# Optimization experiments

Measured on AMD Instinct MI355X. Metric: run time of the kernel, lower is better.

The kernel has to match this reference:

```python
import jax, jax.numpy as jnp
import numpy as np

T, B, S = 32, 64, 64          # tgt_len, batch, src_len
V, E, H, L = 32000, 512, 1024, 2  # vocab, word_vec, rnn_size, layers


def setup_inputs() -> dict:
    key = jax.random.key(0)
    ks = jax.random.split(key, 16)
    s = 0.02
    emb = jax.random.normal(ks[5], (V, E)) * s
    emb = emb.at[0].set(0.0)  # padding_idx=0 row is zero
    return {
        "input": jax.random.randint(ks[0], (T, B), 0, V),
        "h0": jax.random.normal(ks[1], (L, B, H)) * s,
        "c0": jax.random.normal(ks[2], (L, B, H)) * s,
        "context": jax.random.normal(ks[3], (S, B, H)),
        "init_output": jax.random.normal(ks[4], (B, H)) * s,
        "embedding": emb,
        "W_ih0": jax.random.normal(ks[6], (4 * H, E + H)) * s,  # layer0 input = emb + input-feed
        "W_hh0": jax.random.normal(ks[7], (4 * H, H)) * s,
        "b0": jnp.zeros((4 * H,), jnp.float32),
        "W_ih1": jax.random.normal(ks[8], (4 * H, H)) * s,
        "W_hh1": jax.random.normal(ks[9], (4 * H, H)) * s,
        "b1": jnp.zeros((4 * H,), jnp.float32),
        "attn_in_w": jax.random.normal(ks[10], (H, H)) * s,
        "attn_out_w": jax.random.normal(ks[11], (H, 2 * H)) * s,
        "copy_in_w": jax.random.normal(ks[12], (H, H)) * s,
    }


def _lstm_cell(x, h, c, W_ih, W_hh, b):
    g = x @ W_ih.T + h @ W_hh.T + b
    i, f, gg, o = jnp.split(g, 4, axis=-1)  # PyTorch gate order i,f,g,o
    c_new = jax.nn.sigmoid(f) * c + jax.nn.sigmoid(i) * jnp.tanh(gg)
    h_new = jax.nn.sigmoid(o) * jnp.tanh(c_new)
    return h_new, c_new


def _global_attention(in_w, out_w, query, ctx):
    # query: (B,H), ctx: (B,S,H)
    q = query @ in_w.T
    scores = jnp.einsum('bd,bsd->bs', q, ctx)
    a = jax.nn.softmax(scores, axis=-1)
    wctx = jnp.einsum('bs,bsd->bd', a, ctx)
    out = jnp.tanh(jnp.concatenate([wctx, query], axis=-1) @ out_w.T)
    return out, a


def reference(input, h0, c0, context, init_output, embedding,
              W_ih0, W_hh0, b0, W_ih1, W_hh1, b1,
              attn_in_w, attn_out_w, copy_in_w):
    ctx = jnp.transpose(context, (1, 0, 2))  # (B,S,H)
    emb = embedding[input]                    # (T,B,E)

    def step(carry, emb_t):
        h, c, out_feed = carry
        x = jnp.concatenate([emb_t, out_feed], axis=-1)  # input feed
        h0n, c0n = _lstm_cell(x, h[0], c[0], W_ih0, W_hh0, b0)
        h1n, c1n = _lstm_cell(h0n, h[1], c[1], W_ih1, W_hh1, b1)
        out, a_std = _global_attention(attn_in_w, attn_out_w, h1n, ctx)
        # copy attention: only the weights are kept by the original module
        qc = out @ copy_in_w.T
        a_copy = jax.nn.softmax(jnp.einsum('bd,bsd->bs', qc, ctx), axis=-1)
        new_carry = (jnp.stack([h0n, h1n]), jnp.stack([c0n, c1n]), out)
        return new_carry, (out, a_std, a_copy)

    (h_T, c_T, _), (outputs, attn_std, attn_copy) = jax.lax.scan(
        step, (h0, c0, init_output), emb)
    return outputs, (h_T, c_T), attn_std, attn_copy
```

## Files before the change

### kernel.cpp

```cpp
#include <hip/hip_runtime.h>

typedef unsigned short u16;
typedef unsigned int   u32;
typedef __attribute__((ext_vector_type(8))) __bf16 bfrag;
typedef __attribute__((ext_vector_type(4))) float  f32x4;
typedef __attribute__((ext_vector_type(2))) u32    u32x2;
typedef __attribute__((ext_vector_type(4))) u32    u32x4;

#define DEVI static __device__ __forceinline__

#define ST2SC(p, v)    asm volatile("global_store_short %0, %1, off sc0 sc1"   :: "v"(p), "v"(v) : "memory")
#define ST4SC(p, v)    asm volatile("global_store_dword %0, %1, off sc0 sc1"   :: "v"(p), "v"(v) : "memory")
#define ST8SC(p, v)    asm volatile("global_store_dwordx2 %0, %1, off sc0 sc1" :: "v"(p), "v"(v) : "memory")
#define ST16SC(p, v)   asm volatile("global_store_dwordx4 %0, %1, off sc0 sc1" :: "v"(p), "v"(v) : "memory")
#define VMFLUSH()      asm volatile("s_waitcnt vmcnt(0)" ::: "memory")

constexpr long OUT_OFF = 0;
constexpr long HT_OFF  = 2097152;
constexpr long CT_OFF  = 2228224;
constexpr long AS_OFF  = 2359296;
constexpr long AC_OFF  = 2490368;

constexpr long WAO_O   = 0;
constexpr long CTX_O   = 4194304;
constexpr long OFR_O   = 0;
constexpr long H0R_O   = 4194304;
constexpr long H1R_O   = 8388608;
constexpr long WAI_O   = 12582912;
constexpr long WC_O    = 14680064;
constexpr long CTXW_O  = 16777216;
constexpr long CTXWC_O = 25165824;
constexpr long CTXOT_O = 33554432;
constexpr long EBF_O   = 41943040;
constexpr long OF0_O   = 44040192;
constexpr long H00_O   = 44171264;
constexpr long H10_O   = 44302336;
constexpr long AB_O    = 44433408;
constexpr long AFLAG_O = 44957696;
constexpr long BAR_O   = 44965888;

constexpr int W0LDS_O = 0;
constexpr int W1LDS_O = 81920;
constexpr int SCR_O   = 147456;
constexpr int SCR2_O  = 156160;

struct KParams {
  const int* input; const float* h0; const float* c0; const float* context;
  const float* init_output; const float* embedding;
  const float* W_ih0; const float* W_hh0; const float* b0;
  const float* W_ih1; const float* W_hh1; const float* b1;
  const float* attn_in; const float* attn_out; const float* copy_in;
  float* out; char* ws;
};

DEVI float bf2f(u16 u) { u32 x = ((u32)u) << 16; return __builtin_bit_cast(float, x); }
DEVI u16 f2bf(float f) {
  u32 x = __builtin_bit_cast(u32, f);
  u32 r = x + 0x7fffu + ((x >> 16) & 1u);
  return (u16)(r >> 16);
}
DEVI void cvtc_sc(const float* s, char* d) {
  float4 v = *(const float4*)s;
  u32x2 u;
  u[0] = (u32)f2bf(v.x) | ((u32)f2bf(v.y) << 16);
  u[1] = (u32)f2bf(v.z) | ((u32)f2bf(v.w) << 16);
  ST8SC(d, u);
}
DEVI float sigm(float x)  { return 1.f / (1.f + __expf(-x)); }
DEVI float tanh_(float x) { return 1.f - 2.f / (__expf(2.f * x) + 1.f); }
DEVI f32x4 mfma16(bfrag a, bfrag b, f32x4 c) {
  return __builtin_amdgcn_mfma_f32_16x16x32_bf16(a, b, c, 0, 0, 0);
}
DEVI u32 fragoff(int m, int k) {
  return (u32)((((k >> 5) * 4 + (m >> 4)) * 64 + ((k >> 3) & 3) * 16 + (m & 15)) * 16 + (k & 7) * 2);
}
DEVI char* of_slot(char* w, int s) { return w + (s ? OFR_O + (long)(s - 1) * 131072 : OF0_O); }
DEVI char* h0_slot(char* w, int s) { return w + (s ? H0R_O + (long)(s - 1) * 131072 : H00_O); }
DEVI char* h1_slot(char* w, int s) { return w + (s ? H1R_O + (long)(s - 1) * 131072 : H10_O); }

DEVI void pollflags(u32* flags, u32 gen) {
  int t = threadIdx.x;
  for (;;) {
    u32 a = __hip_atomic_load(&flags[t],       __ATOMIC_RELAXED, __HIP_MEMORY_SCOPE_AGENT);
    u32 b = __hip_atomic_load(&flags[64 + t],  __ATOMIC_RELAXED, __HIP_MEMORY_SCOPE_AGENT);
    u32 c = __hip_atomic_load(&flags[128 + t], __ATOMIC_RELAXED, __HIP_MEMORY_SCOPE_AGENT);
    u32 d = __hip_atomic_load(&flags[192 + t], __ATOMIC_RELAXED, __HIP_MEMORY_SCOPE_AGENT);
    if (__all((a >= gen) && (b >= gen) && (c >= gen) && (d >= gen))) break;
  }
}
DEVI void barr_arrive(u32* flags, u32 gen) {
  VMFLUSH();
  __syncthreads();
  if (threadIdx.x == 0)
    __hip_atomic_store(&flags[blockIdx.x], gen, __ATOMIC_RELAXED, __HIP_MEMORY_SCOPE_AGENT);
}
DEVI void barr_wait(u32* flags, u32 gen) {
  u32* bc = flags + 320;
  if (blockIdx.x == 128) {
    if (threadIdx.x < 64) pollflags(flags, gen);
    __syncthreads();
    if (threadIdx.x == 0)
      __hip_atomic_store(bc, gen, __ATOMIC_RELAXED, __HIP_MEMORY_SCOPE_AGENT);
  } else {
    if (threadIdx.x == 0) {
      while (__hip_atomic_load(bc, __ATOMIC_RELAXED, __HIP_MEMORY_SCOPE_AGENT) < gen) {}
    }
  }
  __syncthreads();
  asm volatile("" ::: "memory");
}
DEVI void gsync_fence(u32* flags, u32 gen) {
  __syncthreads();
  if (threadIdx.x == 0) {
    __builtin_amdgcn_fence(__ATOMIC_RELEASE, "agent");
    __hip_atomic_store(&flags[blockIdx.x], gen, __ATOMIC_RELAXED, __HIP_MEMORY_SCOPE_AGENT);
  }
  if (threadIdx.x < 64) pollflags(flags, gen);
  if (threadIdx.x == 0) __builtin_amdgcn_fence(__ATOMIC_ACQUIRE, "agent");
  __syncthreads();
}

template<int N4>
DEVI void gseg(f32x4& acc, const char* Af, int kkA0, int mt, int lane,
               const char* W, int wRowK, int kkW0, int brow, int ke) {
  const u32 sw = (u32)((brow & 7) << 4);
#pragma unroll
  for (int g = 0; g < N4; ++g) {
#pragma unroll
    for (int q = 0; q < 4; ++q) {
      const char* pa = Af + ((((kkA0 + g * 4 + q) * 4 + mt) * 64 + lane) << 4);
      bfrag av = *(const bfrag*)pa;
      int kkW = kkW0 + g * 4 + q;
      u32 off = ((u32)(brow * wRowK + kkW * 32 + ke) * 2) ^ sw;
      acc = mfma16(av, *(const bfrag*)(W + off), acc);
    }
  }
}

DEVI void scr_store(float* scr, int slot, f32x4 acc) {
  const int lane = threadIdx.x & 63;
#pragma unroll
  for (int r = 0; r < 4; ++r)
    scr[slot * 272 + ((lane >> 4) * 4 + r) * 17 + (lane & 15)] = acc[r];
}

DEVI void pointwise64(int bid, const float* scr, const float* bias, float (&cst)[4], char* hfrag) {
  const int m = threadIdx.x;
  const int mt = m >> 4, ml = m & 15;
  u32 hp0 = 0, hp1 = 0;
#pragma unroll
  for (int u = 0; u < 4; ++u) {
    const int j = bid * 4 + u;
    float g0 = scr[(mt*2)*272 + ml*17 + u]      + scr[(mt*2+1)*272 + ml*17 + u]      + bias[j];
    float g1 = scr[(mt*2)*272 + ml*17 + 4 + u]  + scr[(mt*2+1)*272 + ml*17 + 4 + u]  + bias[1024 + j];
    float g2 = scr[(mt*2)*272 + ml*17 + 8 + u]  + scr[(mt*2+1)*272 + ml*17 + 8 + u]  + bias[2048 + j];
    float g3 = scr[(mt*2)*272 + ml*17 + 12 + u] + scr[(mt*2+1)*272 + ml*17 + 12 + u] + bias[3072 + j];
    float cn = sigm(g1) * cst[u] + sigm(g0) * tanh_(g2);
    cst[u] = cn;
    u32 hb = (u32)f2bf(sigm(g3) * tanh_(cn));
    if (u == 0) hp0 = hb; else if (u == 1) hp0 |= hb << 16;
    else if (u == 2) hp1 = hb; else hp1 |= hb << 16;
  }
  u32x2 v; v[0] = hp0; v[1] = hp1;
  ST8SC(hfrag + fragoff(m, bid * 4), v);
}

DEVI void copyattn_step(int b, int tau, const u16* CtxWc, const float* outp,
                        float* xch, float* dout) {
  const int tid = threadIdx.x, lane = tid & 63, w = tid >> 6;
  float ov[16];
  {
    const float4* op = (const float4*)(outp + (long)tau * 65536 + b * 1024 + lane * 16);
#pragma unroll
    for (int i = 0; i < 4; ++i) {
      float4 v = op[i];
      ov[4 * i] = v.x; ov[4 * i + 1] = v.y; ov[4 * i + 2] = v.z; ov[4 * i + 3] = v.w;
    }
  }
  const u16* cwb = CtxWc + (long)b * 65536;
#pragma unroll
  for (int si = 0; si < 8; ++si) {
    int s = w * 8 + si;
    const u32* u = (const u32*)(cwb + (long)s * 1024 + lane * 16);
    float acc = 0.f;
#pragma unroll
    for (int i = 0; i < 8; ++i) {
      u32 x = u[i];
      acc += ov[2 * i] * bf2f((u16)(x & 0xffff));
      acc += ov[2 * i + 1] * bf2f((u16)(x >> 16));
    }
#pragma unroll
    for (int off = 32; off; off >>= 1) acc += __shfl_down(acc, off, 64);
    if (lane == 0) xch[s] = acc;
  }
  __syncthreads();
  if (w == 0) {
    float v = xch[lane];
    float mx = v;
#pragma unroll
    for (int off = 32; off; off >>= 1) mx = fmaxf(mx, __shfl_xor(mx, off, 64));
    float e = __expf(v - mx);
    float sm = e;
#pragma unroll
    for (int off = 32; off; off >>= 1) sm += __shfl_xor(sm, off, 64);
    dout[AC_OFF + (long)tau * 4096 + b * 64 + lane] = e / sm;
  }
}

DEVI void ctxw_gemm(int mt, const u16* Ctx, const u16* Wm, u16* dst) {
  const int tid = threadIdx.x, lane = tid & 63, w = tid >> 6;
  const int arow = mt * 16 + (lane & 15);
  const int ke = (lane >> 4) * 8;
#pragma unroll
  for (int i = 0; i < 8; ++i) {
    int nt = w * 8 + i;
    const u16* A = Ctx + (long)arow * 1024 + ke;
    const u16* B = Wm + (long)(nt * 16 + (lane & 15)) * 1024 + ke;
    f32x4 acc = {0.f, 0.f, 0.f, 0.f};
    for (int kk = 0; kk < 1024; kk += 32)
      acc = mfma16(*(const bfrag*)(A + kk), *(const bfrag*)(B + kk), acc);
#pragma unroll
    for (int r = 0; r < 4; ++r)
      ST2SC((char*)(dst + (long)(mt * 16 + (lane >> 4) * 4 + r) * 1024 + nt * 16 + (lane & 15)),
            (u32)f2bf(acc[r]));
  }
}

DEVI void ctxo_gemm(int bid, const u16* Ctx, const u16* Wao, u16* dst) {
  const int tid = threadIdx.x, lane = tid & 63, w = tid >> 6;
  const int arow = bid * 16 + (lane & 15);
  const int ke = (lane >> 4) * 8;
  const int b = bid >> 2, s0 = (bid & 3) * 16 + (lane >> 4) * 4;
#pragma unroll
  for (int i = 0; i < 8; ++i) {
    int nt = w * 8 + i;
    int j = nt * 16 + (lane & 15);
    const u16* A = Ctx + (long)arow * 1024 + ke;
    const u16* B = Wao + (long)j * 2048 + ke;
    f32x4 acc = {0.f, 0.f, 0.f, 0.f};
    for (int kk = 0; kk < 1024; kk += 32)
      acc = mfma16(*(const bfrag*)(A + kk), *(const bfrag*)(B + kk), acc);
    u32x2 q;
    q[0] = (u32)f2bf(acc[0]) | ((u32)f2bf(acc[1]) << 16);
    q[1] = (u32)f2bf(acc[2]) | ((u32)f2bf(acc[3]) << 16);
    ST8SC((char*)(dst + ((long)(b * 1024 + j) * 64 + s0)), q);
  }
}

__global__ __launch_bounds__(512, 1) void decoder_kernel(KParams p) {
  extern __shared__ char smem[];
  char*  W0   = smem + W0LDS_O;
  char*  W1   = smem + W1LDS_O;
  float* scr  = (float*)(smem + SCR_O);
  float* scr2 = (float*)(smem + SCR2_O);

  char* wsb = p.ws;
  u16* Wao   = (u16*)(wsb + WAO_O);
  u16* Wai   = (u16*)(wsb + WAI_O);
  u16* Wc    = (u16*)(wsb + WC_O);
  u16* Ctx   = (u16*)(wsb + CTX_O);
  u16* CtxW  = (u16*)(wsb + CTXW_O);
  u16* CtxWc = (u16*)(wsb + CTXWC_O);
  u16* CtxOT = (u16*)(wsb + CTXOT_O);
  u32* bar   = (u32*)(wsb + BAR_O);

  const int bid = blockIdx.x, tid = threadIdx.x;
  const int lane = tid & 63, w = tid >> 6;
  const long gtid = (long)bid * 512 + tid, NT = 256l * 512;
  u32 gen = 1;

  {
    float* tile = (float*)smem;
    for (int pass = 0; pass < 2; ++pass) {
      const float* src = pass ? p.copy_in : p.attn_in;
      u16* dst = pass ? Wc : Wai;
      int tr = bid >> 4, tc = bid & 15;
      {
        int r = tid >> 3, c = (tid & 7) * 8;
        const float4* s4 = (const float4*)(src + (long)(tr * 64 + r) * 1024 + tc * 64 + c);
        float4 a = s4[0], b = s4[1];
        float* tp = tile + r * 69 + c;
        tp[0] = a.x; tp[1] = a.y; tp[2] = a.z; tp[3] = a.w;
        tp[4] = b.x; tp[5] = b.y; tp[6] = b.z; tp[7] = b.w;
      }
      __syncthreads();
      {
        int r2 = tid >> 3, c2 = (tid & 7) * 8;
        u32x4 q;
#pragma unroll
        for (int i = 0; i < 4; ++i) {
          float lo = tile[(c2 + 2 * i) * 69 + r2];
          float hi = tile[(c2 + 2 * i + 1) * 69 + r2];
          q[i] = (u32)f2bf(lo) | ((u32)f2bf(hi) << 16);
        }
        ST16SC((char*)(dst + (long)(tc * 64 + r2) * 1024 + tr * 64 + c2), q);
      }
      __syncthreads();
    }
  }

  for (int i = tid; i < 5120; i += 512) {
    int row = i / 320, k = (i % 320) * 8;
    int R = (row >> 2) * 1024 + bid * 4 + (row & 3);
    const float* src = (k < 1536) ? (p.W_ih0 + (long)R * 1536 + k)
                                  : (p.W_hh0 + (long)R * 1024 + (k - 1536));
    float4 a = *(const float4*)src, b = *(const float4*)(src + 4);
    uint4 q;
    q.x = (u32)f2bf(a.x) | ((u32)f2bf(a.y) << 16);
    q.y = (u32)f2bf(a.z) | ((u32)f2bf(a.w) << 16);
    q.z = (u32)f2bf(b.x) | ((u32)f2bf(b.y) << 16);
    q.w = (u32)f2bf(b.z) | ((u32)f2bf(b.w) << 16);
    u32 off = ((u32)(row * 2560 + k) * 2) ^ ((u32)((row & 7) << 4));
    *(uint4*)(W0 + off) = q;
  }
  for (int i = tid; i < 4096; i += 512) {
    int row = i / 256, k = (i % 256) * 8;
    int R = (row >> 2) * 1024 + bid * 4 + (row & 3);
    const float* src = (k < 1024) ? (p.W_ih1 + (long)R * 1024 + k)
                                  : (p.W_hh1 + (long)R * 1024 + (k - 1024));
    float4 a = *(const float4*)src, b = *(const float4*)(src + 4);
    uint4 q;
    q.x = (u32)f2bf(a.x) | ((u32)f2bf(a.y) << 16);
    q.y = (u32)f2bf(a.z) | ((u32)f2bf(a.w) << 16);
    q.z = (u32)f2bf(b.x) | ((u32)f2bf(b.y) << 16);
    q.w = (u32)f2bf(b.z) | ((u32)f2bf(b.w) << 16);
    u32 off = ((u32)(row * 2048 + k) * 2) ^ ((u32)((row & 7) << 4));
    *(uint4*)(W1 + off) = q;
  }

  for (long i = gtid; i < 524288; i += NT) cvtc_sc(p.attn_out + i * 4, (char*)(Wao + i * 4));
  for (long i = gtid; i < 1048576; i += NT) {
    long b = i >> 14, s = (i >> 8) & 63, kq = i & 255;
    cvtc_sc(p.context + ((s * 64 + b) * 1024 + kq * 4), (char*)(Ctx + i * 4));
  }
  for (long i = gtid; i < 262144; i += NT) {
    long row = i >> 7; long t = row >> 6, b = row & 63;
    long k0 = (i & 127) * 4;
    long tok = p.input[row];
    cvtc_sc(p.embedding + tok * 512 + k0, wsb + EBF_O + t * 65536 + fragoff((int)b, (int)k0));
  }
  for (long i = gtid; i < 16384; i += NT) {
    long b = i >> 8, k0 = (i & 255) * 4;
    cvtc_sc(p.init_output + i * 4, of_slot(wsb, 0) + fragoff((int)b, (int)k0));
  }
  for (long i = gtid; i < 32768; i += NT) {
    long l = i >> 14, rem = i & 16383, b = rem >> 8, k0 = (rem & 255) * 4;
    cvtc_sc(p.h0 + i * 4, (l ? h1_slot(wsb, 0) : h0_slot(wsb, 0)) + fragoff((int)b, (int)k0));
  }

  float cR0[4] = {0.f, 0.f, 0.f, 0.f}, cR1[4] = {0.f, 0.f, 0.f, 0.f};
  if (tid < 64) {
#pragma unroll
    for (int u = 0; u < 4; ++u) {
      cR0[u] = p.c0[(long)tid * 1024 + bid * 4 + u];
      cR1[u] = p.c0[65536 + (long)tid * 1024 + bid * 4 + u];
    }
  }

  gsync_fence(bar, gen); ++gen;

  ctxw_gemm(bid, Ctx, Wai, CtxW);
  ctxw_gemm(bid, Ctx, Wc, CtxWc);
  ctxo_gemm(bid, Ctx, Wao, CtxOT);
  gsync_fence(bar, gen); ++gen;

  const int xcd = bid & 7, idx = bid >> 3;
  const int ntP4 = xcd * 8 + (idx & 7), mtP4 = idx >> 3;
  const int browP4 = ntP4 * 16 + (lane & 15);
  const int ke_ = (lane >> 4) * 8;
  bfrag waoreg[4];
#pragma unroll
  for (int q = 0; q < 4; ++q)
    waoreg[q] = *(const bfrag*)(Wao + (long)browP4 * 2048 + 1024 + (w * 4 + q) * 32 + ke_);

  const int mt_ = w & 3, kh_ = w >> 2;
  const int brow_ = lane & 15;

  f32x4 accP1 = {0.f, 0.f, 0.f, 0.f}, accP2;
  {
    const char* E0  = wsb + EBF_O;
    const char* H0p = h0_slot(wsb, 0);
    if (kh_ == 0) {
      gseg<2>(accP1, E0,  0,  mt_, lane, W0, 2560, 0,  brow_, ke_);
      gseg<4>(accP1, H0p, 0,  mt_, lane, W0, 2560, 48, brow_, ke_);
    } else {
      gseg<2>(accP1, E0,  8,  mt_, lane, W0, 2560, 8,  brow_, ke_);
      gseg<4>(accP1, H0p, 16, mt_, lane, W0, 2560, 64, brow_, ke_);
    }
  }

  for (int t = 0; t < 32; ++t) {
    const char* OFc   = of_slot(wsb, t);
    char*       Hb0cF = h0_slot(wsb, t + 1);
    char*       Hb1cF = h1_slot(wsb, t + 1);
    const char* Hb1pF = h1_slot(wsb, t);
    char*       ABt   = wsb + AB_O + (long)t * 16384;

    {
      f32x4 acc = accP1;
      if (kh_ == 0) gseg<4>(acc, OFc, 0,  mt_, lane, W0, 2560, 16, brow_, ke_);
      else          gseg<4>(acc, OFc, 16, mt_, lane, W0, 2560, 32, brow_, ke_);
      scr_store(scr, mt_ * 2 + kh_, acc);
      __syncthreads();
      if (tid < 64) pointwise64(bid, scr, p.b0, cR0, Hb0cF);
    }
    barr_arrive(bar, gen);
    accP2 = f32x4{0.f, 0.f, 0.f, 0.f};
    if (kh_ == 0) gseg<4>(accP2, Hb1pF, 0,  mt_, lane, W1, 2048, 32, brow_, ke_);
    else          gseg<4>(accP2, Hb1pF, 16, mt_, lane, W1, 2048, 48, brow_, ke_);
    barr_wait(bar, gen); ++gen;

    {
      f32x4 acc = accP2;
      if (kh_ == 0) gseg<4>(acc, Hb0cF, 0,  mt_, lane, W1, 2048, 0,  brow_, ke_);
      else          gseg<4>(acc, Hb0cF, 16, mt_, lane, W1, 2048, 16, brow_, ke_);
      scr_store(scr, mt_ * 2 + kh_, acc);
      __syncthreads();
      if (tid < 64) pointwise64(bid, scr, p.b1, cR1, Hb1cF);
    }
    barr_arrive(bar, gen);
    accP1 = f32x4{0.f, 0.f, 0.f, 0.f};
    {
      const char* En = wsb + EBF_O + (long)((t + 1) & 31) * 65536;
      if (kh_ == 0) {
        gseg<2>(accP1, En,    0,  mt_, lane, W0, 2560, 0,  brow_, ke_);
        gseg<2>(accP1, Hb0cF, 0,  mt_, lane, W0, 2560, 48, brow_, ke_);
      } else {
        gseg<2>(accP1, En,    8,  mt_, lane, W0, 2560, 8,  brow_, ke_);
        gseg<2>(accP1, Hb0cF, 16, mt_, lane, W0, 2560, 64, brow_, ke_);
      }
    }
    barr_wait(bar, gen); ++gen;

    if (bid < 64) {
      const int b = bid;
      float h1v[16];
      {
        int k0 = lane * 16;
        const u32* hp0 = (const u32*)(Hb1cF + fragoff(b, k0));
        const u32* hp1 = (const u32*)(Hb1cF + fragoff(b, k0 + 8));
        u32 uu[8] = {hp0[0], hp0[1], hp0[2], hp0[3], hp1[0], hp1[1], hp1[2], hp1[3]};
#pragma unroll
        for (int i = 0; i < 8; ++i) {
          h1v[2 * i]     = bf2f((u16)(uu[i] & 0xffff));
          h1v[2 * i + 1] = bf2f((u16)(uu[i] >> 16));
        }
      }
      const u16* cwb = CtxW + (long)b * 65536;
#pragma unroll
      for (int si = 0; si < 8; ++si) {
        int s = w * 8 + si;
        const u32* u = (const u32*)(cwb + (long)s * 1024 + lane * 16);
        float acc = 0.f;
#pragma unroll
        for (int i = 0; i < 8; ++i) {
          u32 x = u[i];
          acc += h1v[2 * i] * bf2f((u16)(x & 0xffff));
          acc += h1v[2 * i + 1] * bf2f((u16)(x >> 16));
        }
#pragma unroll
        for (int off = 32; off; off >>= 1) acc += __shfl_down(acc, off, 64);
        if (lane == 0) scr2[s] = acc;
      }
      __syncthreads();
      if (w == 0) {
        float v = scr2[lane];
        float mx = v;
#pragma unroll
        for (int off = 32; off; off >>= 1) mx = fmaxf(mx, __shfl_xor(mx, off, 64));
        float e = __expf(v - mx);
        float sm = e;
#pragma unroll
        for (int off = 32; off; off >>= 1) sm += __shfl_xor(sm, off, 64);
        float a = e / sm;
        ST4SC(ABt + (u32)(b * 64 + lane) * 4, __builtin_bit_cast(u32, a));
        ST4SC((char*)(p.out + AS_OFF + (long)t * 4096 + b * 64 + lane), __builtin_bit_cast(u32, a));
        VMFLUSH();
        if (lane == 0)
          ST4SC(wsb + AFLAG_O + ((u32)t * 64 + b) * 4, 1u);
      }
      __syncthreads();
    }
    {
      const char* bp = Hb1cF;
      bfrag h0_ = *(const bfrag*)(bp + ((((w * 4 + 0) * 4 + mtP4) * 64 + lane) << 4));
      bfrag h1_ = *(const bfrag*)(bp + ((((w * 4 + 1) * 4 + mtP4) * 64 + lane) << 4));
      bfrag h2_ = *(const bfrag*)(bp + ((((w * 4 + 2) * 4 + mtP4) * 64 + lane) << 4));
      bfrag h3_ = *(const bfrag*)(bp + ((((w * 4 + 3) * 4 + mtP4) * 64 + lane) << 4));
      f32x4 a4 = {0.f, 0.f, 0.f, 0.f};
      a4 = mfma16(h0_, waoreg[0], a4);
      a4 = mfma16(h1_, waoreg[1], a4);
      a4 = mfma16(h2_, waoreg[2], a4);
      a4 = mfma16(h3_, waoreg[3], a4);
      scr_store(scr, w, a4);
    }
    if (bid >= 192 && t > 0)
      copyattn_step(bid - 192, t - 1, CtxWc, p.out, scr2, p.out);

    {
      const int pair = tid >> 1, half = tid & 1;
      const int m_l = pair >> 4, j_l = pair & 15;
      const int b = mtP4 * 16 + m_l, j = ntP4 * 16 + j_l;
      u32 cpr[16];
      {
        const u32* cp = (const u32*)(CtxOT + ((long)(b * 1024 + j) * 64 + half * 32));
#pragma unroll
        for (int i = 0; i < 16; ++i) cpr[i] = cp[i];
      }
      if (tid < 16) {
        const u32* fp = (const u32*)(wsb + AFLAG_O + ((u32)t * 64 + mtP4 * 16 + tid) * 4);
        while (__hip_atomic_load(fp, __ATOMIC_RELAXED, __HIP_MEMORY_SCOPE_AGENT) == 0) {}
      }
      __syncthreads();
      {
        int b0i = tid >> 6, s0i = tid & 63;
        int b1i = (tid + 512) >> 6;
        scr2[tid]       = *(const float*)(ABt + (u32)(((mtP4 * 16 + b0i) * 64 + s0i)) * 4);
        scr2[tid + 512] = *(const float*)(ABt + (u32)(((mtP4 * 16 + b1i) * 64 + s0i)) * 4);
      }
      __syncthreads();
      const float* al = scr2 + m_l * 64 + half * 32;
      float acc = 0.f;
#pragma unroll
      for (int i = 0; i < 16; ++i) {
        u32 x = cpr[i];
        acc += al[2 * i] * bf2f((u16)(x & 0xffff));
        acc += al[2 * i + 1] * bf2f((u16)(x >> 16));
      }
      float v = acc + __shfl_xor(acc, 1, 64);
      if (half == 0) {
        float h1p = 0.f;
#pragma unroll
        for (int q = 0; q < 8; ++q) h1p += scr[q * 272 + m_l * 17 + j_l];
        v = tanh_(v + h1p);
        ST4SC((char*)(p.out + (long)t * 65536 + b * 1024 + j), __builtin_bit_cast(u32, v));
        u32 hv = (u32)f2bf(v);
        ST2SC(of_slot(wsb, t + 1) + fragoff(b, j), hv);
      }
    }
    barr_arrive(bar, gen);
    if (kh_ == 0) gseg<2>(accP1, Hb0cF, 8,  mt_, lane, W0, 2560, 56, brow_, ke_);
    else          gseg<2>(accP1, Hb0cF, 24, mt_, lane, W0, 2560, 72, brow_, ke_);
    barr_wait(bar, gen); ++gen;
  }

  if (tid < 64) {
#pragma unroll
    for (int u = 0; u < 4; ++u) {
      int j = bid * 4 + u;
      p.out[CT_OFF + (long)tid * 1024 + j]         = cR0[u];
      p.out[CT_OFF + 65536 + (long)tid * 1024 + j] = cR1[u];
    }
  }
  if (tid < 256) {
    int u = tid >> 6, m = tid & 63, j = bid * 4 + u;
    u16 a0 = *(const u16*)(h0_slot(wsb, 32) + fragoff(m, j));
    u16 a1 = *(const u16*)(h1_slot(wsb, 32) + fragoff(m, j));
    p.out[HT_OFF + (long)m * 1024 + j]         = bf2f(a0);
    p.out[HT_OFF + 65536 + (long)m * 1024 + j] = bf2f(a1);
  }

  if (bid >= 192) {
    __syncthreads();
    copyattn_step(bid - 192, 31, CtxWc, p.out, scr2, p.out);
  }
}

extern "C" void kernel_launch(void* const* d_in, const int* in_sizes, int n_in,
                              void* d_out, int out_size, void* d_ws, size_t ws_size,
                              hipStream_t stream) {
  KParams p;
  p.input       = (const int*)d_in[0];
  p.h0          = (const float*)d_in[1];
  p.c0          = (const float*)d_in[2];
  p.context     = (const float*)d_in[3];
  p.init_output = (const float*)d_in[4];
  p.embedding   = (const float*)d_in[5];
  p.W_ih0       = (const float*)d_in[6];
  p.W_hh0       = (const float*)d_in[7];
  p.b0          = (const float*)d_in[8];
  p.W_ih1       = (const float*)d_in[9];
  p.W_hh1       = (const float*)d_in[10];
  p.b1          = (const float*)d_in[11];
  p.attn_in     = (const float*)d_in[12];
  p.attn_out    = (const float*)d_in[13];
  p.copy_in     = (const float*)d_in[14];
  p.out         = (float*)d_out;
  p.ws          = (char*)d_ws;

  (void)hipFuncSetAttribute((const void*)decoder_kernel,
                            hipFuncAttributeMaxDynamicSharedMemorySize, 160256);
  (void)hipMemsetAsync((char*)d_ws + AB_O, 0, 534528, stream);
  void* args[] = { &p };
  (void)hipLaunchCooperativeKernel((void*)decoder_kernel, dim3(256), dim3(512),
                                   args, 160256, stream);
}
```

Baseline: 1.534 ms.

## Replace grid-wide barriers with per-chunk dataflow counters and dedicated attention blocks

Removes the per-step global arrive/wait barriers. In their place, each block increments per-chunk counters after producing h0, h1 and output-feed slices, and consumers poll only the chunks they need. The output-projection tiles are redistributed so the first 64 blocks handle attention scores exclusively and the other blocks take one or two projection tiles each. The software pipelining of the next step's embedding and hidden partial GEMMs across barriers is dropped. This trades global barrier latency for finer-grained waits, which may let layers and steps overlap, at the cost of more atomics, polling traffic and some load imbalance from the dual-tile blocks.

```diff
diff --git a/kernel.cpp b/kernel.cpp
--- a/kernel.cpp
+++ b/kernel.cpp
@@ -37,7 +37,10 @@
 constexpr long H10_O   = 44302336;
 constexpr long AB_O    = 44433408;
 constexpr long AFLAG_O = 44957696;
-constexpr long BAR_O   = 44965888;
+constexpr long H0C_O   = 44965888;
+constexpr long H1C_O   = 45033472;
+constexpr long OFC_O   = 45101056;
+constexpr long BAR_O   = 45168640;
 
 constexpr int W0LDS_O = 0;
 constexpr int W1LDS_O = 81920;
@@ -78,6 +81,20 @@
 DEVI char* h0_slot(char* w, int s) { return w + (s ? H0R_O + (long)(s - 1) * 131072 : H00_O); }
 DEVI char* h1_slot(char* w, int s) { return w + (s ? H1R_O + (long)(s - 1) * 131072 : H10_O); }
 
+DEVI u32* cntb(char* w, long base, int slot) { return (u32*)(w + base + (long)slot * 2048); }
+DEVI void cnt_add(u32* c) {
+  (void)__hip_atomic_fetch_add(c, 1u, __ATOMIC_RELAXED, __HIP_MEMORY_SCOPE_AGENT);
+}
+template<int N>
+DEVI void poll_chunks(const u32* base, int c0) {
+  const int lane = threadIdx.x & 63;
+  const u32* p = base + (u32)(c0 + (lane & (N - 1))) * 16;
+  for (;;) {
+    u32 v = __hip_atomic_load(p, __ATOMIC_RELAXED, __HIP_MEMORY_SCOPE_AGENT);
+    if (__all(v >= 8u)) break;
+  }
+}
+
 DEVI void pollflags(u32* flags, u32 gen) {
   int t = threadIdx.x;
   for (;;) {
@@ -87,27 +104,6 @@
     u32 d = __hip_atomic_load(&flags[192 + t], __ATOMIC_RELAXED, __HIP_MEMORY_SCOPE_AGENT);
     if (__all((a >= gen) && (b >= gen) && (c >= gen) && (d >= gen))) break;
   }
-}
-DEVI void barr_arrive(u32* flags, u32 gen) {
-  VMFLUSH();
-  __syncthreads();
-  if (threadIdx.x == 0)
-    __hip_atomic_store(&flags[blockIdx.x], gen, __ATOMIC_RELAXED, __HIP_MEMORY_SCOPE_AGENT);
-}
-DEVI void barr_wait(u32* flags, u32 gen) {
-  u32* bc = flags + 320;
-  if (blockIdx.x == 128) {
-    if (threadIdx.x < 64) pollflags(flags, gen);
-    __syncthreads();
-    if (threadIdx.x == 0)
-      __hip_atomic_store(bc, gen, __ATOMIC_RELAXED, __HIP_MEMORY_SCOPE_AGENT);
-  } else {
-    if (threadIdx.x == 0) {
-      while (__hip_atomic_load(bc, __ATOMIC_RELAXED, __HIP_MEMORY_SCOPE_AGENT) < gen) {}
-    }
-  }
-  __syncthreads();
-  asm volatile("" ::: "memory");
 }
 DEVI void gsync_fence(u32* flags, u32 gen) {
   __syncthreads();
@@ -225,7 +221,6 @@
             (u32)f2bf(acc[r]));
   }
 }
-
 DEVI void ctxo_gemm(int bid, const u16* Ctx, const u16* Wao, u16* dst) {
   const int tid = threadIdx.x, lane = tid & 63, w = tid >> 6;
   const int arow = bid * 16 + (lane & 15);
@@ -245,6 +240,63 @@
     q[1] = (u32)f2bf(acc[2]) | ((u32)f2bf(acc[3]) << 16);
     ST8SC((char*)(dst + ((long)(b * 1024 + j) * 64 + s0)), q);
   }
+}
+
+DEVI void p4_tile(int t, int mt, int nt, const bfrag (&waoreg)[4],
+                  const char* H1n, char* wsb, const u16* CtxOT,
+                  float* scr, float* scr2, float* outp) {
+  const int tid = threadIdx.x, lane = tid & 63, w = tid >> 6;
+  poll_chunks<4>(cntb(wsb, H1C_O, t + 1), w * 4);
+  {
+    bfrag h0_ = *(const bfrag*)(H1n + ((((w * 4 + 0) * 4 + mt) * 64 + lane) << 4));
+    bfrag h1_ = *(const bfrag*)(H1n + ((((w * 4 + 1) * 4 + mt) * 64 + lane) << 4));
+    bfrag h2_ = *(const bfrag*)(H1n + ((((w * 4 + 2) * 4 + mt) * 64 + lane) << 4));
+    bfrag h3_ = *(const bfrag*)(H1n + ((((w * 4 + 3) * 4 + mt) * 64 + lane) << 4));
+    f32x4 a4 = {0.f, 0.f, 0.f, 0.f};
+    a4 = mfma16(h0_, waoreg[0], a4);
+    a4 = mfma16(h1_, waoreg[1], a4);
+    a4 = mfma16(h2_, waoreg[2], a4);
+    a4 = mfma16(h3_, waoreg[3], a4);
+    scr_store(scr, w, a4);
+  }
+  char* ABt = wsb + AB_O + (long)t * 16384;
+  if (tid < 16) {
+    const u32* fp = (const u32*)(wsb + AFLAG_O + ((u32)t * 64 + mt * 16 + tid) * 4);
+    while (__hip_atomic_load(fp, __ATOMIC_RELAXED, __HIP_MEMORY_SCOPE_AGENT) == 0) {}
+  }
+  __syncthreads();
+  {
+    int b0i = tid >> 6, s0i = tid & 63;
+    int b1i = (tid + 512) >> 6;
+    scr2[tid]       = *(const float*)(ABt + (u32)(((mt * 16 + b0i) * 64 + s0i)) * 4);
+    scr2[tid + 512] = *(const float*)(ABt + (u32)(((mt * 16 + b1i) * 64 + s0i)) * 4);
+  }
+  __syncthreads();
+  const int pair = tid >> 1, half = tid & 1;
+  const int m_l = pair >> 4, j_l = pair & 15;
+  const int b = mt * 16 + m_l, j = nt * 16 + j_l;
+  const u32* cp = (const u32*)(CtxOT + ((long)(b * 1024 + j) * 64 + half * 32));
+  const float* al = scr2 + m_l * 64 + half * 32;
+  float acc = 0.f;
+#pragma unroll
+  for (int i = 0; i < 16; ++i) {
+    u32 x = cp[i];
+    acc += al[2 * i] * bf2f((u16)(x & 0xffff));
+    acc += al[2 * i + 1] * bf2f((u16)(x >> 16));
+  }
+  float v = acc + __shfl_xor(acc, 1, 64);
+  if (half == 0) {
+    float h1p = 0.f;
+#pragma unroll
+    for (int q = 0; q < 8; ++q) h1p += scr[q * 272 + m_l * 17 + j_l];
+    v = tanh_(v + h1p);
+    ST4SC((char*)(outp + (long)t * 65536 + b * 1024 + j), __builtin_bit_cast(u32, v));
+    u32 hv = (u32)f2bf(v);
+    ST2SC(of_slot(wsb, t + 1) + fragoff(b, j), hv);
+  }
+  VMFLUSH();
+  __syncthreads();
+  if (tid == 0) cnt_add(cntb(wsb, OFC_O, t + 1) + (nt >> 1) * 16);
 }
 
 __global__ __launch_bounds__(512, 1) void decoder_kernel(KParams p) {
@@ -364,81 +416,75 @@
   ctxo_gemm(bid, Ctx, Wao, CtxOT);
   gsync_fence(bar, gen); ++gen;
 
-  const int xcd = bid & 7, idx = bid >> 3;
-  const int ntP4 = xcd * 8 + (idx & 7), mtP4 = idx >> 3;
-  const int browP4 = ntP4 * 16 + (lane & 15);
+  const bool isP3 = bid < 64;
+  const int tbase = bid - 64;
+  const bool dual = !isP3 && tbase < 64;
+  int mtP4 = 0, ntP4 = 0;
+  if (!isP3) {
+    int vidx = tbase >> 3;
+    mtP4 = vidx >> 3;
+    ntP4 = (tbase & 7) * 8 + (vidx & 7);
+  }
   const int ke_ = (lane >> 4) * 8;
   bfrag waoreg[4];
-#pragma unroll
-  for (int q = 0; q < 4; ++q)
-    waoreg[q] = *(const bfrag*)(Wao + (long)browP4 * 2048 + 1024 + (w * 4 + q) * 32 + ke_);
+  if (!isP3) {
+    const int browP4 = ntP4 * 16 + (lane & 15);
+#pragma unroll
+    for (int q = 0; q < 4; ++q)
+      waoreg[q] = *(const bfrag*)(Wao + (long)browP4 * 2048 + 1024 + (w * 4 + q) * 32 + ke_);
+  }
 
   const int mt_ = w & 3, kh_ = w >> 2;
   const int brow_ = lane & 15;
 
-  f32x4 accP1 = {0.f, 0.f, 0.f, 0.f}, accP2;
-  {
-    const char* E0  = wsb + EBF_O;
-    const char* H0p = h0_slot(wsb, 0);
-    if (kh_ == 0) {
-      gseg<2>(accP1, E0,  0,  mt_, lane, W0, 2560, 0,  brow_, ke_);
-      gseg<4>(accP1, H0p, 0,  mt_, lane, W0, 2560, 48, brow_, ke_);
-    } else {
-      gseg<2>(accP1, E0,  8,  mt_, lane, W0, 2560, 8,  brow_, ke_);
-      gseg<4>(accP1, H0p, 16, mt_, lane, W0, 2560, 64, brow_, ke_);
-    }
-  }
-
   for (int t = 0; t < 32; ++t) {
-    const char* OFc   = of_slot(wsb, t);
-    char*       Hb0cF = h0_slot(wsb, t + 1);
-    char*       Hb1cF = h1_slot(wsb, t + 1);
-    const char* Hb1pF = h1_slot(wsb, t);
-    char*       ABt   = wsb + AB_O + (long)t * 16384;
+    const char* OFc = of_slot(wsb, t);
+    const char* H0c = h0_slot(wsb, t);
+    char*       H0n = h0_slot(wsb, t + 1);
+    char*       H1n = h1_slot(wsb, t + 1);
+    const char* H1c = h1_slot(wsb, t);
 
     {
-      f32x4 acc = accP1;
+      f32x4 acc = {0.f, 0.f, 0.f, 0.f};
+      const char* En = wsb + EBF_O + (long)t * 65536;
+      if (kh_ == 0) gseg<2>(acc, En, 0, mt_, lane, W0, 2560, 0, brow_, ke_);
+      else          gseg<2>(acc, En, 8, mt_, lane, W0, 2560, 8, brow_, ke_);
+      if (t > 0) poll_chunks<16>(cntb(wsb, OFC_O, t), kh_ * 16);
       if (kh_ == 0) gseg<4>(acc, OFc, 0,  mt_, lane, W0, 2560, 16, brow_, ke_);
       else          gseg<4>(acc, OFc, 16, mt_, lane, W0, 2560, 32, brow_, ke_);
+      if (t > 0) poll_chunks<16>(cntb(wsb, H0C_O, t), kh_ * 16);
+      if (kh_ == 0) gseg<4>(acc, H0c, 0,  mt_, lane, W0, 2560, 48, brow_, ke_);
+      else          gseg<4>(acc, H0c, 16, mt_, lane, W0, 2560, 64, brow_, ke_);
       scr_store(scr, mt_ * 2 + kh_, acc);
       __syncthreads();
-      if (tid < 64) pointwise64(bid, scr, p.b0, cR0, Hb0cF);
-    }
-    barr_arrive(bar, gen);
-    accP2 = f32x4{0.f, 0.f, 0.f, 0.f};
-    if (kh_ == 0) gseg<4>(accP2, Hb1pF, 0,  mt_, lane, W1, 2048, 32, brow_, ke_);
-    else          gseg<4>(accP2, Hb1pF, 16, mt_, lane, W1, 2048, 48, brow_, ke_);
-    barr_wait(bar, gen); ++gen;
+      if (tid < 64) { pointwise64(bid, scr, p.b0, cR0, H0n); VMFLUSH(); }
+      __syncthreads();
+      if (tid == 0) cnt_add(cntb(wsb, H0C_O, t + 1) + (bid >> 3) * 16);
+    }
 
     {
-      f32x4 acc = accP2;
-      if (kh_ == 0) gseg<4>(acc, Hb0cF, 0,  mt_, lane, W1, 2048, 0,  brow_, ke_);
-      else          gseg<4>(acc, Hb0cF, 16, mt_, lane, W1, 2048, 16, brow_, ke_);
+      f32x4 acc = {0.f, 0.f, 0.f, 0.f};
+      poll_chunks<16>(cntb(wsb, H0C_O, t + 1), kh_ * 16);
+      if (kh_ == 0) gseg<4>(acc, H0n, 0,  mt_, lane, W1, 2048, 0,  brow_, ke_);
+      else          gseg<4>(acc, H0n, 16, mt_, lane, W1, 2048, 16, brow_, ke_);
+      if (t > 0) poll_chunks<16>(cntb(wsb, H1C_O, t), kh_ * 16);
+      if (kh_ == 0) gseg<4>(acc, H1c, 0,  mt_, lane, W1, 2048, 32, brow_, ke_);
+      else          gseg<4>(acc, H1c, 16, mt_, lane, W1, 2048, 48, brow_, ke_);
       scr_store(scr, mt_ * 2 + kh_, acc);
       __syncthreads();
-      if (tid < 64) pointwise64(bid, scr, p.b1, cR1, Hb1cF);
-    }
-    barr_arrive(bar, gen);
-    accP1 = f32x4{0.f, 0.f, 0.f, 0.f};
-    {
-      const char* En = wsb + EBF_O + (long)((t + 1) & 31) * 65536;
-      if (kh_ == 0) {
-        gseg<2>(accP1, En,    0,  mt_, lane, W0, 2560, 0,  brow_, ke_);
-        gseg<2>(accP1, Hb0cF, 0,  mt_, lane, W0, 2560, 48, brow_, ke_);
-      } else {
-        gseg<2>(accP1, En,    8,  mt_, lane, W0, 2560, 8,  brow_, ke_);
-        gseg<2>(accP1, Hb0cF, 16, mt_, lane, W0, 2560, 64, brow_, ke_);
-      }
-    }
-    barr_wait(bar, gen); ++gen;
-
-    if (bid < 64) {
+      if (tid < 64) { pointwise64(bid, scr, p.b1, cR1, H1n); VMFLUSH(); }
+      __syncthreads();
+      if (tid == 0) cnt_add(cntb(wsb, H1C_O, t + 1) + (bid >> 3) * 16);
+    }
+
+    if (isP3) {
       const int b = bid;
+      poll_chunks<32>(cntb(wsb, H1C_O, t + 1), 0);
       float h1v[16];
       {
         int k0 = lane * 16;
-        const u32* hp0 = (const u32*)(Hb1cF + fragoff(b, k0));
-        const u32* hp1 = (const u32*)(Hb1cF + fragoff(b, k0 + 8));
+        const u32* hp0 = (const u32*)(H1n + fragoff(b, k0));
+        const u32* hp1 = (const u32*)(H1n + fragoff(b, k0 + 8));
         u32 uu[8] = {hp0[0], hp0[1], hp0[2], hp0[3], hp1[0], hp1[1], hp1[2], hp1[3]};
 #pragma unroll
         for (int i = 0; i < 8; ++i) {
@@ -473,77 +519,32 @@
 #pragma unroll
         for (int off = 32; off; off >>= 1) sm += __shfl_xor(sm, off, 64);
         float a = e / sm;
-        ST4SC(ABt + (u32)(b * 64 + lane) * 4, __builtin_bit_cast(u32, a));
+        ST4SC(wsb + AB_O + (long)t * 16384 + (u32)(b * 64 + lane) * 4, __builtin_bit_cast(u32, a));
         ST4SC((char*)(p.out + AS_OFF + (long)t * 4096 + b * 64 + lane), __builtin_bit_cast(u32, a));
         VMFLUSH();
         if (lane == 0)
           ST4SC(wsb + AFLAG_O + ((u32)t * 64 + b) * 4, 1u);
       }
       __syncthreads();
-    }
-    {
-      const char* bp = Hb1cF;
-      bfrag h0_ = *(const bfrag*)(bp + ((((w * 4 + 0) * 4 + mtP4) * 64 + lane) << 4));
-      bfrag h1_ = *(const bfrag*)(bp + ((((w * 4 + 1) * 4 + mtP4) * 64 + lane) << 4));
-      bfrag h2_ = *(const bfrag*)(bp + ((((w * 4 + 2) * 4 + mtP4) * 64 + lane) << 4));
-      bfrag h3_ = *(const bfrag*)(bp + ((((w * 4 + 3) * 4 + mtP4) * 64 + lane) << 4));
-      f32x4 a4 = {0.f, 0.f, 0.f, 0.f};
-      a4 = mfma16(h0_, waoreg[0], a4);
-      a4 = mfma16(h1_, waoreg[1], a4);
-      a4 = mfma16(h2_, waoreg[2], a4);
-      a4 = mfma16(h3_, waoreg[3], a4);
-      scr_store(scr, w, a4);
-    }
-    if (bid >= 192 && t > 0)
-      copyattn_step(bid - 192, t - 1, CtxWc, p.out, scr2, p.out);
-
-    {
-      const int pair = tid >> 1, half = tid & 1;
-      const int m_l = pair >> 4, j_l = pair & 15;
-      const int b = mtP4 * 16 + m_l, j = ntP4 * 16 + j_l;
-      u32 cpr[16];
-      {
-        const u32* cp = (const u32*)(CtxOT + ((long)(b * 1024 + j) * 64 + half * 32));
-#pragma unroll
-        for (int i = 0; i < 16; ++i) cpr[i] = cp[i];
-      }
-      if (tid < 16) {
-        const u32* fp = (const u32*)(wsb + AFLAG_O + ((u32)t * 64 + mtP4 * 16 + tid) * 4);
-        while (__hip_atomic_load(fp, __ATOMIC_RELAXED, __HIP_MEMORY_SCOPE_AGENT) == 0) {}
-      }
-      __syncthreads();
-      {
-        int b0i = tid >> 6, s0i = tid & 63;
-        int b1i = (tid + 512) >> 6;
-        scr2[tid]       = *(const float*)(ABt + (u32)(((mtP4 * 16 + b0i) * 64 + s0i)) * 4);
-        scr2[tid + 512] = *(const float*)(ABt + (u32)(((mtP4 * 16 + b1i) * 64 + s0i)) * 4);
-      }
-      __syncthreads();
-      const float* al = scr2 + m_l * 64 + half * 32;
-      float acc = 0.f;
-#pragma unroll
-      for (int i = 0; i < 16; ++i) {
-        u32 x = cpr[i];
-        acc += al[2 * i] * bf2f((u16)(x & 0xffff));
-        acc += al[2 * i + 1] * bf2f((u16)(x >> 16));
-      }
-      float v = acc + __shfl_xor(acc, 1, 64);
-      if (half == 0) {
-        float h1p = 0.f;
-#pragma unroll
-        for (int q = 0; q < 8; ++q) h1p += scr[q * 272 + m_l * 17 + j_l];
-        v = tanh_(v + h1p);
-        ST4SC((char*)(p.out + (long)t * 65536 + b * 1024 + j), __builtin_bit_cast(u32, v));
-        u32 hv = (u32)f2bf(v);
-        ST2SC(of_slot(wsb, t + 1) + fragoff(b, j), hv);
-      }
-    }
-    barr_arrive(bar, gen);
-    if (kh_ == 0) gseg<2>(accP1, Hb0cF, 8,  mt_, lane, W0, 2560, 56, brow_, ke_);
-    else          gseg<2>(accP1, Hb0cF, 24, mt_, lane, W0, 2560, 72, brow_, ke_);
-    barr_wait(bar, gen); ++gen;
-  }
-
+    } else {
+      if (bid >= 192 && t > 0) {
+        poll_chunks<32>(cntb(wsb, OFC_O, t), 0);
+        copyattn_step(bid - 192, t - 1, CtxWc, p.out, scr2, p.out);
+        __syncthreads();
+      }
+      p4_tile(t, mtP4, ntP4, waoreg, H1n, wsb, CtxOT, scr, scr2, p.out);
+      if (dual) {
+        __syncthreads();
+        p4_tile(t, mtP4 + 3, ntP4, waoreg, H1n, wsb, CtxOT, scr, scr2, p.out);
+      }
+    }
+  }
+
+  if (w == 0) {
+    poll_chunks<32>(cntb(wsb, H0C_O, 32), 0);
+    poll_chunks<32>(cntb(wsb, H1C_O, 32), 0);
+  }
+  __syncthreads();
   if (tid < 64) {
 #pragma unroll
     for (int u = 0; u < 4; ++u) {
@@ -561,6 +562,7 @@
   }
 
   if (bid >= 192) {
+    poll_chunks<32>(cntb(wsb, OFC_O, 32), 0);
     __syncthreads();
     copyattn_step(bid - 192, 31, CtxWc, p.out, scr2, p.out);
   }
@@ -590,7 +592,7 @@
 
   (void)hipFuncSetAttribute((const void*)decoder_kernel,
                             hipFuncAttributeMaxDynamicSharedMemorySize, 160256);
-  (void)hipMemsetAsync((char*)d_ws + AB_O, 0, 534528, stream);
+  (void)hipMemsetAsync((char*)d_ws + AB_O, 0, 737280, stream);
   void* args[] = { &p };
   (void)hipLaunchCooperativeKernel((void*)decoder_kernel, dim3(256), dim3(512),
                                    args, 160256, stream);
```

Result: slower. 2.016 ms (+31.4%).

## Offload output-projection tiles from attention-score blocks to dual-tile blocks

Applied to the files above, without the earlier changes.

The 64 blocks that compute attention scores and softmax no longer also compute an output-projection tile. Their mt=0 tiles, which share the same weight columns, now run as a second tile in blocks 64-127. The output-projection tile code moves into a helper, and the copy-attention step gets an explicit barrier before it. The aim is to take the score blocks off the output critical path so they finish the softmax sooner. In exchange, half of the other blocks do twice the output-projection work per step, which could lengthen the step.

```diff
diff --git a/kernel.cpp b/kernel.cpp
--- a/kernel.cpp
+++ b/kernel.cpp
@@ -225,7 +225,6 @@
             (u32)f2bf(acc[r]));
   }
 }
-
 DEVI void ctxo_gemm(int bid, const u16* Ctx, const u16* Wao, u16* dst) {
   const int tid = threadIdx.x, lane = tid & 63, w = tid >> 6;
   const int arow = bid * 16 + (lane & 15);
@@ -244,6 +243,64 @@
     q[0] = (u32)f2bf(acc[0]) | ((u32)f2bf(acc[1]) << 16);
     q[1] = (u32)f2bf(acc[2]) | ((u32)f2bf(acc[3]) << 16);
     ST8SC((char*)(dst + ((long)(b * 1024 + j) * 64 + s0)), q);
+  }
+}
+
+DEVI void p4_tile(int t, int mt, int nt, const bfrag (&waoreg)[4],
+                  const char* H1n, char* wsb, const u16* CtxOT,
+                  float* scr, float* scr2, float* outp) {
+  const int tid = threadIdx.x, lane = tid & 63, w = tid >> 6;
+  {
+    bfrag h0_ = *(const bfrag*)(H1n + ((((w * 4 + 0) * 4 + mt) * 64 + lane) << 4));
+    bfrag h1_ = *(const bfrag*)(H1n + ((((w * 4 + 1) * 4 + mt) * 64 + lane) << 4));
+    bfrag h2_ = *(const bfrag*)(H1n + ((((w * 4 + 2) * 4 + mt) * 64 + lane) << 4));
+    bfrag h3_ = *(const bfrag*)(H1n + ((((w * 4 + 3) * 4 + mt) * 64 + lane) << 4));
+    f32x4 a4 = {0.f, 0.f, 0.f, 0.f};
+    a4 = mfma16(h0_, waoreg[0], a4);
+    a4 = mfma16(h1_, waoreg[1], a4);
+    a4 = mfma16(h2_, waoreg[2], a4);
+    a4 = mfma16(h3_, waoreg[3], a4);
+    scr_store(scr, w, a4);
+  }
+  const int pair = tid >> 1, half = tid & 1;
+  const int m_l = pair >> 4, j_l = pair & 15;
+  const int b = mt * 16 + m_l, j = nt * 16 + j_l;
+  u32 cpr[16];
+  {
+    const u32* cp = (const u32*)(CtxOT + ((long)(b * 1024 + j) * 64 + half * 32));
+#pragma unroll
+    for (int i = 0; i < 16; ++i) cpr[i] = cp[i];
+  }
+  char* ABt = wsb + AB_O + (long)t * 16384;
+  if (tid < 16) {
+    const u32* fp = (const u32*)(wsb + AFLAG_O + ((u32)t * 64 + mt * 16 + tid) * 4);
+    while (__hip_atomic_load(fp, __ATOMIC_RELAXED, __HIP_MEMORY_SCOPE_AGENT) == 0) {}
+  }
+  __syncthreads();
+  {
+    int b0i = tid >> 6, s0i = tid & 63;
+    int b1i = (tid + 512) >> 6;
+    scr2[tid]       = *(const float*)(ABt + (u32)(((mt * 16 + b0i) * 64 + s0i)) * 4);
+    scr2[tid + 512] = *(const float*)(ABt + (u32)(((mt * 16 + b1i) * 64 + s0i)) * 4);
+  }
+  __syncthreads();
+  const float* al = scr2 + m_l * 64 + half * 32;
+  float acc = 0.f;
+#pragma unroll
+  for (int i = 0; i < 16; ++i) {
+    u32 x = cpr[i];
+    acc += al[2 * i] * bf2f((u16)(x & 0xffff));
+    acc += al[2 * i + 1] * bf2f((u16)(x >> 16));
+  }
+  float v = acc + __shfl_xor(acc, 1, 64);
+  if (half == 0) {
+    float h1p = 0.f;
+#pragma unroll
+    for (int q = 0; q < 8; ++q) h1p += scr[q * 272 + m_l * 17 + j_l];
+    v = tanh_(v + h1p);
+    ST4SC((char*)(outp + (long)t * 65536 + b * 1024 + j), __builtin_bit_cast(u32, v));
+    u32 hv = (u32)f2bf(v);
+    ST2SC(of_slot(wsb, t + 1) + fragoff(b, j), hv);
   }
 }
 
@@ -364,14 +421,22 @@
   ctxo_gemm(bid, Ctx, Wao, CtxOT);
   gsync_fence(bar, gen); ++gen;
 
-  const int xcd = bid & 7, idx = bid >> 3;
-  const int ntP4 = xcd * 8 + (idx & 7), mtP4 = idx >> 3;
-  const int browP4 = ntP4 * 16 + (lane & 15);
+  const bool isP3 = bid < 64;
+  const bool dual = (bid >= 64) && (bid < 128);
+  int mtP4 = 0, ntP4 = 0;
+  if (!isP3) {
+    const int xcd = bid & 7, idx = bid >> 3;
+    ntP4 = xcd * 8 + (idx & 7);
+    mtP4 = idx >> 3;
+  }
   const int ke_ = (lane >> 4) * 8;
   bfrag waoreg[4];
-#pragma unroll
-  for (int q = 0; q < 4; ++q)
-    waoreg[q] = *(const bfrag*)(Wao + (long)browP4 * 2048 + 1024 + (w * 4 + q) * 32 + ke_);
+  if (!isP3) {
+    const int browP4 = ntP4 * 16 + (lane & 15);
+#pragma unroll
+    for (int q = 0; q < 4; ++q)
+      waoreg[q] = *(const bfrag*)(Wao + (long)browP4 * 2048 + 1024 + (w * 4 + q) * 32 + ke_);
+  }
 
   const int mt_ = w & 3, kh_ = w >> 2;
   const int brow_ = lane & 15;
@@ -432,7 +497,7 @@
     }
     barr_wait(bar, gen); ++gen;
 
-    if (bid < 64) {
+    if (isP3) {
       const int b = bid;
       float h1v[16];
       {
@@ -480,62 +545,15 @@
           ST4SC(wsb + AFLAG_O + ((u32)t * 64 + b) * 4, 1u);
       }
       __syncthreads();
-    }
-    {
-      const char* bp = Hb1cF;
-      bfrag h0_ = *(const bfrag*)(bp + ((((w * 4 + 0) * 4 + mtP4) * 64 + lane) << 4));
-      bfrag h1_ = *(const bfrag*)(bp + ((((w * 4 + 1) * 4 + mtP4) * 64 + lane) << 4));
-      bfrag h2_ = *(const bfrag*)(bp + ((((w * 4 + 2) * 4 + mtP4) * 64 + lane) << 4));
-      bfrag h3_ = *(const bfrag*)(bp + ((((w * 4 + 3) * 4 + mtP4) * 64 + lane) << 4));
-      f32x4 a4 = {0.f, 0.f, 0.f, 0.f};
-      a4 = mfma16(h0_, waoreg[0], a4);
-      a4 = mfma16(h1_, waoreg[1], a4);
-      a4 = mfma16(h2_, waoreg[2], a4);
-      a4 = mfma16(h3_, waoreg[3], a4);
-      scr_store(scr, w, a4);
-    }
-    if (bid >= 192 && t > 0)
-      copyattn_step(bid - 192, t - 1, CtxWc, p.out, scr2, p.out);
-
-    {
-      const int pair = tid >> 1, half = tid & 1;
-      const int m_l = pair >> 4, j_l = pair & 15;
-      const int b = mtP4 * 16 + m_l, j = ntP4 * 16 + j_l;
-      u32 cpr[16];
-      {
-        const u32* cp = (const u32*)(CtxOT + ((long)(b * 1024 + j) * 64 + half * 32));
-#pragma unroll
-        for (int i = 0; i < 16; ++i) cpr[i] = cp[i];
-      }
-      if (tid < 16) {
-        const u32* fp = (const u32*)(wsb + AFLAG_O + ((u32)t * 64 + mtP4 * 16 + tid) * 4);
-        while (__hip_atomic_load(fp, __ATOMIC_RELAXED, __HIP_MEMORY_SCOPE_AGENT) == 0) {}
-      }
-      __syncthreads();
-      {
-        int b0i = tid >> 6, s0i = tid & 63;
-        int b1i = (tid + 512) >> 6;
-        scr2[tid]       = *(const float*)(ABt + (u32)(((mtP4 * 16 + b0i) * 64 + s0i)) * 4);
-        scr2[tid + 512] = *(const float*)(ABt + (u32)(((mtP4 * 16 + b1i) * 64 + s0i)) * 4);
-      }
-      __syncthreads();
-      const float* al = scr2 + m_l * 64 + half * 32;
-      float acc = 0.f;
-#pragma unroll
-      for (int i = 0; i < 16; ++i) {
-        u32 x = cpr[i];
-        acc += al[2 * i] * bf2f((u16)(x & 0xffff));
-        acc += al[2 * i + 1] * bf2f((u16)(x >> 16));
-      }
-      float v = acc + __shfl_xor(acc, 1, 64);
-      if (half == 0) {
-        float h1p = 0.f;
-#pragma unroll
-        for (int q = 0; q < 8; ++q) h1p += scr[q * 272 + m_l * 17 + j_l];
-        v = tanh_(v + h1p);
-        ST4SC((char*)(p.out + (long)t * 65536 + b * 1024 + j), __builtin_bit_cast(u32, v));
-        u32 hv = (u32)f2bf(v);
-        ST2SC(of_slot(wsb, t + 1) + fragoff(b, j), hv);
+    } else {
+      if (bid >= 192 && t > 0) {
+        copyattn_step(bid - 192, t - 1, CtxWc, p.out, scr2, p.out);
+        __syncthreads();
+      }
+      p4_tile(t, mtP4, ntP4, waoreg, Hb1cF, wsb, CtxOT, scr, scr2, p.out);
+      if (dual) {
+        __syncthreads();
+        p4_tile(t, 0, ntP4, waoreg, Hb1cF, wsb, CtxOT, scr, scr2, p.out);
       }
     }
     barr_arrive(bar, gen);
```

After: 1.659 ms. 1.08x slower.
